# Kernel tuning notes

Measured on AMD Instinct MI355X. Metric: run time of the kernel, lower is better.

Reference implementation:

```python
import jax, jax.numpy as jnp
import numpy as np

B, L, D = 2, 1024, 1024
H = 16
NL = 2
DFF = 4 * D
EPS = 1e-5
W_SCALE = 0.02


def rmsnorm(x, w):
    # x * rsqrt(mean(x^2, -1) + eps) * w   (computed in fp32 as in the torch code)
    xf = x.astype(jnp.float32)
    n = xf * jax.lax.rsqrt(jnp.mean(xf * xf, axis=-1, keepdims=True) + EPS)
    return n.astype(x.dtype) * w


def setup_inputs() -> dict:
    key = jax.random.key(0)
    ks = jax.random.split(key, 10)
    x = jax.random.normal(ks[0], (B, L, D), dtype=jnp.float32)
    # torch nn.Linear weight layout: [out_features, in_features]; y = x @ W.T + b
    qw = jax.random.normal(ks[1], (NL, D, D), dtype=jnp.float32) * W_SCALE
    kw = jax.random.normal(ks[2], (NL, D, D), dtype=jnp.float32) * W_SCALE
    vw = jax.random.normal(ks[3], (NL, D, D), dtype=jnp.float32) * W_SCALE
    ow = jax.random.normal(ks[4], (NL, D, D), dtype=jnp.float32) * W_SCALE
    pn_w = jnp.ones((NL, D), dtype=jnp.float32)
    ln_w = jnp.ones((NL, D), dtype=jnp.float32)
    fc_w = jax.random.normal(ks[5], (NL, DFF, D), dtype=jnp.float32) * W_SCALE
    fc2_w = jax.random.normal(ks[6], (NL, D, DFF), dtype=jnp.float32) * W_SCALE
    fc2_b = jnp.zeros((NL, D), dtype=jnp.float32)
    return {"x": x, "qw": qw, "kw": kw, "vw": vw, "ow": ow,
            "pn_w": pn_w, "ln_w": ln_w, "fc_w": fc_w, "fc2_w": fc2_w, "fc2_b": fc2_b}


def reference(x, qw, kw, vw, ow, pn_w, ln_w, fc_w, fc2_w, fc2_b):
    d = D // H
    for i in range(NL):
        # --- LinearAttention block (dropout=0 -> identity) ---
        h = rmsnorm(x, pn_w[i])                                   # [B,L,D]
        Q = (h @ qw[i].T).reshape(B, L, H, d)
        K = (h @ kw[i].T).reshape(B, L, H, d)
        V = (h @ vw[i].T).reshape(B, L, H, d)
        # outer-product state per position, cumulated over L (causal linear attn)
        W = jnp.einsum('blhd,blhe->blhde', K, V)                  # [B,L,H,d,d]
        W = jnp.cumsum(W, axis=1)
        a = jnp.einsum('blhd,blhde->blhe', Q, W).reshape(B, L, D)
        x = x + a @ ow[i].T
        # --- MLP block ---
        m = rmsnorm(x, ln_w[i])
        f = jax.nn.gelu(m @ fc_w[i].T, approximate=False)         # torch nn.GELU default = exact
        x = x + f @ fc2_w[i].T + fc2_b[i]
    return x
```

## Files before the change

kernel.cpp:

```cpp
#include <hip/hip_runtime.h>

#define BB 2
#define LL 1024
#define DD 1024
#define HH 16
#define HD 64
#define DFFN 4096
#define MM (BB*LL)
#define QS 3072

using u16 = unsigned short;
typedef __bf16 bf16x8 __attribute__((ext_vector_type(8)));
typedef float f32x4 __attribute__((ext_vector_type(4)));

__device__ __forceinline__ float b2f(u16 u) {
  union { unsigned int i; float f; } v; v.i = ((unsigned int)u) << 16; return v.f;
}
__device__ __forceinline__ u16 f2b(float f) {
  union { float f; unsigned int i; } v; v.f = f;
  unsigned int x = v.i;
  return (u16)((x + 0x7fffu + ((x >> 16) & 1u)) >> 16);
}
__device__ __forceinline__ float gelu_exact(float x) {
  return 0.5f * x * (1.0f + erff(x * 0.70710678118654752f));
}
__device__ __forceinline__ void gl2lds16(const void* g, void* l) {
  __builtin_amdgcn_global_load_lds((const __attribute__((address_space(1))) void*)g,
                                   (__attribute__((address_space(3))) void*)l, 16, 0, 0);
}

__global__ __launch_bounds__(256) void castw_kernel(const float* __restrict__ in,
                                                    u16* __restrict__ out, int n8) {
  int i = blockIdx.x * 256 + threadIdx.x;
  if (i >= n8) return;
  const float4 a = reinterpret_cast<const float4*>(in)[2 * i];
  const float4 b = reinterpret_cast<const float4*>(in)[2 * i + 1];
  uint4 o;
  o.x = (unsigned)f2b(a.x) | ((unsigned)f2b(a.y) << 16);
  o.y = (unsigned)f2b(a.z) | ((unsigned)f2b(a.w) << 16);
  o.z = (unsigned)f2b(b.x) | ((unsigned)f2b(b.y) << 16);
  o.w = (unsigned)f2b(b.z) | ((unsigned)f2b(b.w) << 16);
  reinterpret_cast<uint4*>(out)[i] = o;
}
__global__ __launch_bounds__(256) void castw3_kernel(const float* __restrict__ s0,
                                                     const float* __restrict__ s1,
                                                     const float* __restrict__ s2,
                                                     u16* __restrict__ out, int n8) {
  int i = blockIdx.x * 256 + threadIdx.x;
  if (i >= n8) return;
  const float* in = (blockIdx.y == 0) ? s0 : (blockIdx.y == 1) ? s1 : s2;
  u16* dst = out + (size_t)blockIdx.y * n8 * 8;
  const float4 a = reinterpret_cast<const float4*>(in)[2 * i];
  const float4 b = reinterpret_cast<const float4*>(in)[2 * i + 1];
  uint4 o;
  o.x = (unsigned)f2b(a.x) | ((unsigned)f2b(a.y) << 16);
  o.y = (unsigned)f2b(a.z) | ((unsigned)f2b(a.w) << 16);
  o.z = (unsigned)f2b(b.x) | ((unsigned)f2b(b.y) << 16);
  o.w = (unsigned)f2b(b.z) | ((unsigned)f2b(b.w) << 16);
  reinterpret_cast<uint4*>(dst)[i] = o;
}

__global__ __launch_bounds__(256) void init_out_kernel(float* __restrict__ out,
                                                       const float* __restrict__ resid,
                                                       const float* __restrict__ bias) {
  const int i = blockIdx.x * 256 + threadIdx.x;
  float4 v = reinterpret_cast<const float4*>(resid)[i];
  if (bias != nullptr) {
    const float4 bv = *reinterpret_cast<const float4*>(bias + ((i * 4) & (DD - 1)));
    v.x += bv.x; v.y += bv.y; v.z += bv.z; v.w += bv.w;
  }
  reinterpret_cast<float4*>(out)[i] = v;
}

__global__ __launch_bounds__(256) void rmsnorm_kernel(const float* __restrict__ x,
                                                      const float* __restrict__ w,
                                                      u16* __restrict__ out) {
  const int row = blockIdx.x, t = threadIdx.x;
  const float4 v = reinterpret_cast<const float4*>(x + (size_t)row * DD)[t];
  float ss = v.x*v.x + v.y*v.y + v.z*v.z + v.w*v.w;
  #pragma unroll
  for (int o = 32; o > 0; o >>= 1) ss += __shfl_down(ss, o);
  __shared__ float red[4];
  if ((t & 63) == 0) red[t >> 6] = ss;
  __syncthreads();
  const float inv = rsqrtf((red[0] + red[1] + red[2] + red[3]) * (1.0f / DD) + 1e-5f);
  const float4 wv = reinterpret_cast<const float4*>(w)[t];
  ushort4 o;
  o.x = f2b(v.x * inv * wv.x);
  o.y = f2b(v.y * inv * wv.y);
  o.z = f2b(v.z * inv * wv.z);
  o.w = f2b(v.w * inv * wv.w);
  reinterpret_cast<ushort4*>(out + (size_t)row * DD)[t] = o;
}

template<int ROWS, int NT>
__device__ __forceinline__ void dma32(const u16* __restrict__ g, int r0, int K, int kt,
                                      int t, u16* lds) {
  #pragma unroll
  for (int i = 0; i < ROWS * 4 / NT; i++) {
    const int c = i * NT + t;
    gl2lds16(g + (size_t)(r0 + (c >> 2)) * K + kt + (c & 3) * 8, &lds[c * 8]);
  }
}
__device__ __forceinline__ void mfma_tile32(const u16* Asb, const u16* Bsb,
                                            int wm, int wn, int fr, int fq, f32x4 acc[4][4]) {
  bf16x8 af[4], bfv[4];
  #pragma unroll
  for (int i = 0; i < 4; i++)
    af[i] = *reinterpret_cast<const bf16x8*>(&Asb[(wm + i * 16 + fr) * 32 + fq * 8]);
  #pragma unroll
  for (int j = 0; j < 4; j++)
    bfv[j] = *reinterpret_cast<const bf16x8*>(&Bsb[(wn + j * 16 + fr) * 32 + fq * 8]);
  #pragma unroll
  for (int i = 0; i < 4; i++)
    #pragma unroll
    for (int j = 0; j < 4; j++)
      acc[i][j] = __builtin_amdgcn_mfma_f32_16x16x32_bf16(af[i], bfv[j], acc[i][j], 0, 0, 0);
}

template<int BM, int BN, int ACT>
__global__ __launch_bounds__((BM/64)*(BN/64)*64)
void mfma_gemm(const u16* __restrict__ A, const u16* __restrict__ Wb,
               u16* __restrict__ Cb, int N, int K) {
  constexpr int WCOLS = BN / 64;
  constexpr int NW = (BM / 64) * WCOLS;
  constexpr int NT = NW * 64;
  __shared__ u16 As[BM * 32];
  __shared__ u16 Bs[BN * 32];
  const int t = threadIdx.x;
  const int lane = t & 63, w = t >> 6;
  const int wm = (w / WCOLS) * 64, wn = (w % WCOLS) * 64;
  const int m0 = blockIdx.y * BM, n0 = blockIdx.x * BN;
  const int fr = lane & 15, fq = lane >> 4;

  f32x4 acc[4][4] = {};
  for (int kt = 0; kt < K; kt += 32) {
    dma32<BM, NT>(A, m0, K, kt, t, As);
    dma32<BN, NT>(Wb, n0, K, kt, t, Bs);
    __syncthreads();
    mfma_tile32(As, Bs, wm, wn, fr, fq, acc);
    __syncthreads();
  }

  #pragma unroll
  for (int i = 0; i < 4; i++)
    #pragma unroll
    for (int j = 0; j < 4; j++)
      #pragma unroll
      for (int r = 0; r < 4; r++) {
        const int row = m0 + wm + i * 16 + fq * 4 + r;
        const int col = n0 + wn + j * 16 + fr;
        float val = acc[i][j][r];
        if (ACT == 1) val = gelu_exact(val);
        Cb[(size_t)row * N + col] = f2b(val);
      }
}

template<int SPLIT>
__global__ __launch_bounds__(128)
void mfma_gemm_sk(const u16* __restrict__ A, const u16* __restrict__ Wb,
                  float* __restrict__ Co, int N, int K) {
  constexpr int BM = 128, BN = 64, NT = 128;
  __shared__ u16 As[BM * 32];
  __shared__ u16 Bs[BN * 32];
  const int t = threadIdx.x;
  const int lane = t & 63, w = t >> 6;
  const int wm = w * 64, wn = 0;
  const int m0 = blockIdx.y * BM, n0 = blockIdx.x * BN;
  const int fr = lane & 15, fq = lane >> 4;
  const int Kc = K / SPLIT, k0 = blockIdx.z * Kc, kend = k0 + Kc;

  f32x4 acc[4][4] = {};
  for (int kt = k0; kt < kend; kt += 32) {
    dma32<BM, NT>(A, m0, K, kt, t, As);
    dma32<BN, NT>(Wb, n0, K, kt, t, Bs);
    __syncthreads();
    mfma_tile32(As, Bs, wm, wn, fr, fq, acc);
    __syncthreads();
  }

  #pragma unroll
  for (int i = 0; i < 4; i++)
    #pragma unroll
    for (int j = 0; j < 4; j++)
      #pragma unroll
      for (int r = 0; r < 4; r++) {
        const int row = m0 + wm + i * 16 + fq * 4 + r;
        const int col = n0 + wn + j * 16 + fr;
        unsafeAtomicAdd(&Co[(size_t)row * N + col], acc[i][j][r]);
      }
}

__global__ __launch_bounds__(256) void kv_trans(const u16* __restrict__ QKV,
                                                u16* __restrict__ Kt, u16* __restrict__ Vt) {
  __shared__ u16 T[64][72];
  const int tile = blockIdx.x;
  const int h2 = blockIdx.y;
  const int b = blockIdx.z;
  const int h = h2 & 15, which = h2 >> 4;
  const int t = threadIdx.x;
  const int pos = t >> 2, d0 = (t & 3) * 16;
  const u16* src = QKV + ((size_t)(b * LL) + tile * 64 + pos) * QS + 1024 + which * 1024 + h * HD + d0;
  union { uint4 u[2]; u16 s[16]; } pk;
  pk.u[0] = reinterpret_cast<const uint4*>(src)[0];
  pk.u[1] = reinterpret_cast<const uint4*>(src)[1];
  #pragma unroll
  for (int j = 0; j < 16; j++) T[d0 + j][pos] = pk.s[j];
  __syncthreads();
  const int d = t >> 2, p0 = (t & 3) * 16;
  u16* dst = (which ? Vt : Kt) + ((size_t)(b * HH + h) * HD + d) * LL + tile * 64 + p0;
  union { uint4 u[2]; u16 s[16]; } ok;
  #pragma unroll
  for (int j = 0; j < 16; j++) ok.s[j] = T[d][p0 + j];
  reinterpret_cast<uint4*>(dst)[0] = ok.u[0];
  reinterpret_cast<uint4*>(dst)[1] = ok.u[1];
}

__global__ __launch_bounds__(256) void attn_phase1(const u16* __restrict__ QKV,
                                                   const u16* __restrict__ Kt,
                                                   const u16* __restrict__ Vt,
                                                   u16* __restrict__ Oa,
                                                   u16* __restrict__ Slt) {
  __shared__ u16 Ss[4][16][64];
  const int tile = blockIdx.x, h = blockIdx.y, b = blockIdx.z;
  const int t = threadIdx.x, lane = t & 63, w = t >> 6;
  const int fr = lane & 15, fq = lane >> 4;
  const size_t tok0 = (size_t)(b * LL + tile * 64);
  const size_t bh = (size_t)(b * HH + h);
  const u16* Qb  = QKV + tok0 * QS + h * HD;
  const u16* Kb  = Qb + 1024;
  const u16* Ktb = Kt + bh * (HD * LL) + tile * 64;
  const u16* Vtb = Vt + bh * (HD * LL) + tile * 64;

  bf16x8 aq[2], bk[4][2];
  #pragma unroll
  for (int kh = 0; kh < 2; kh++)
    aq[kh] = *reinterpret_cast<const bf16x8*>(Qb + (size_t)(16*w + fr) * QS + kh*32 + fq*8);
  #pragma unroll
  for (int n4 = 0; n4 < 4; n4++)
    #pragma unroll
    for (int kh = 0; kh < 2; kh++)
      bk[n4][kh] = *reinterpret_cast<const bf16x8*>(Kb + (size_t)(16*n4 + fr) * QS + kh*32 + fq*8);
  f32x4 sacc[4] = {};
  #pragma unroll
  for (int n4 = 0; n4 < 4; n4++) {
    sacc[n4] = __builtin_amdgcn_mfma_f32_16x16x32_bf16(aq[0], bk[n4][0], sacc[n4], 0, 0, 0);
    sacc[n4] = __builtin_amdgcn_mfma_f32_16x16x32_bf16(aq[1], bk[n4][1], sacc[n4], 0, 0, 0);
  }
  #pragma unroll
  for (int n4 = 0; n4 < 4; n4++)
    #pragma unroll
    for (int r = 0; r < 4; r++) {
      const bool keep = (16*w + 4*fq + r) >= (16*n4 + fr);
      Ss[w][4*fq + r][16*n4 + fr] = keep ? f2b(sacc[n4][r]) : (u16)0;
    }
  __syncthreads();

  bf16x8 va[2], kt[4][2];
  #pragma unroll
  for (int kh = 0; kh < 2; kh++)
    va[kh] = *reinterpret_cast<const bf16x8*>(Vtb + (size_t)(16*w + fr) * LL + kh*32 + fq*8);
  #pragma unroll
  for (int n4 = 0; n4 < 4; n4++)
    #pragma unroll
    for (int kh = 0; kh < 2; kh++)
      kt[n4][kh] = *reinterpret_cast<const bf16x8*>(Ktb + (size_t)(16*n4 + fr) * LL + kh*32 + fq*8);
  f32x4 lacc[4] = {};
  #pragma unroll
  for (int n4 = 0; n4 < 4; n4++) {
    lacc[n4] = __builtin_amdgcn_mfma_f32_16x16x32_bf16(va[0], kt[n4][0], lacc[n4], 0, 0, 0);
    lacc[n4] = __builtin_amdgcn_mfma_f32_16x16x32_bf16(va[1], kt[n4][1], lacc[n4], 0, 0, 0);
  }
  u16* So = Slt + (bh * 16 + tile) * 4096;
  #pragma unroll
  for (int n4 = 0; n4 < 4; n4++)
    #pragma unroll
    for (int r = 0; r < 4; r++)
      So[(size_t)(16*w + 4*fq + r) * 64 + 16*n4 + fr] = f2b(lacc[n4][r]);

  bf16x8 sa[2], vb[4][2];
  #pragma unroll
  for (int kh = 0; kh < 2; kh++)
    sa[kh] = *reinterpret_cast<const bf16x8*>(&Ss[w][fr][kh*32 + fq*8]);
  #pragma unroll
  for (int n4 = 0; n4 < 4; n4++)
    #pragma unroll
    for (int kh = 0; kh < 2; kh++)
      vb[n4][kh] = *reinterpret_cast<const bf16x8*>(Vtb + (size_t)(16*n4 + fr) * LL + kh*32 + fq*8);
  f32x4 oacc[4] = {};
  #pragma unroll
  for (int n4 = 0; n4 < 4; n4++) {
    oacc[n4] = __builtin_amdgcn_mfma_f32_16x16x32_bf16(sa[0], vb[n4][0], oacc[n4], 0, 0, 0);
    oacc[n4] = __builtin_amdgcn_mfma_f32_16x16x32_bf16(sa[1], vb[n4][1], oacc[n4], 0, 0, 0);
  }
  u16* Ob = Oa + (tok0 + 16*w) * DD + h * HD;
  #pragma unroll
  for (int n4 = 0; n4 < 4; n4++)
    #pragma unroll
    for (int r = 0; r < 4; r++)
      Ob[(size_t)(4*fq + r) * DD + 16*n4 + fr] = f2b(oacc[n4][r]);
}

__global__ __launch_bounds__(256) void attn_phase2(const u16* __restrict__ Slt,
                                                   u16* __restrict__ Wc) {
  const int rg = blockIdx.x, h = blockIdx.y, b = blockIdx.z;
  const size_t base = ((size_t)((b * HH + h) * 16)) * 4096 + rg * 512 + threadIdx.x * 2;
  float r0 = 0.f, r1 = 0.f;
  for (int tl = 0; tl < 16; tl++) {
    const size_t p = base + (size_t)tl * 4096;
    const unsigned d = *reinterpret_cast<const unsigned*>(Slt + p);
    *reinterpret_cast<unsigned*>(Wc + p) = (unsigned)f2b(r0) | ((unsigned)f2b(r1) << 16);
    r0 += b2f((u16)(d & 0xffff));
    r1 += b2f((u16)(d >> 16));
  }
}

__global__ __launch_bounds__(256) void attn_phase3(const u16* __restrict__ QKV,
                                                   const u16* __restrict__ Wc,
                                                   u16* __restrict__ Oa) {
  const int tile = blockIdx.x, h = blockIdx.y, b = blockIdx.z;
  const int t = threadIdx.x, lane = t & 63, w = t >> 6;
  const int fr = lane & 15, fq = lane >> 4;
  const size_t tok0 = (size_t)(b * LL + tile * 64);
  const size_t bh = (size_t)(b * HH + h);
  const u16* Qb = QKV + tok0 * QS + h * HD;
  const u16* Wb = Wc + (bh * 16 + tile) * 4096;

  bf16x8 aq[2], wb[4][2];
  #pragma unroll
  for (int kh = 0; kh < 2; kh++)
    aq[kh] = *reinterpret_cast<const bf16x8*>(Qb + (size_t)(16*w + fr) * QS + kh*32 + fq*8);
  #pragma unroll
  for (int n4 = 0; n4 < 4; n4++)
    #pragma unroll
    for (int kh = 0; kh < 2; kh++)
      wb[n4][kh] = *reinterpret_cast<const bf16x8*>(Wb + (size_t)(16*n4 + fr) * 64 + kh*32 + fq*8);
  f32x4 oacc[4] = {};
  #pragma unroll
  for (int n4 = 0; n4 < 4; n4++) {
    oacc[n4] = __builtin_amdgcn_mfma_f32_16x16x32_bf16(aq[0], wb[n4][0], oacc[n4], 0, 0, 0);
    oacc[n4] = __builtin_amdgcn_mfma_f32_16x16x32_bf16(aq[1], wb[n4][1], oacc[n4], 0, 0, 0);
  }
  u16* Ob = Oa + (tok0 + 16*w) * DD + h * HD;
  #pragma unroll
  for (int n4 = 0; n4 < 4; n4++)
    #pragma unroll
    for (int r = 0; r < 4; r++) {
      const size_t idx = (size_t)(4*fq + r) * DD + 16*n4 + fr;
      Ob[idx] = f2b(b2f(Ob[idx]) + oacc[n4][r]);
    }
}

extern "C" void kernel_launch(void* const* d_in, const int* in_sizes, int n_in,
                              void* d_out, int out_size, void* d_ws, size_t ws_size,
                              hipStream_t stream) {
  const float* x_in = (const float*)d_in[0];
  const float* qw   = (const float*)d_in[1];
  const float* kw   = (const float*)d_in[2];
  const float* vw   = (const float*)d_in[3];
  const float* ow   = (const float*)d_in[4];
  const float* pn   = (const float*)d_in[5];
  const float* ln   = (const float*)d_in[6];
  const float* fcw  = (const float*)d_in[7];
  const float* fc2w = (const float*)d_in[8];
  const float* fc2b = (const float*)d_in[9];

  char* ws = (char*)d_ws;
  u16* wbuf = (u16*)ws;
  u16* slt  = (u16*)ws;
  u16* wcum = (u16*)(ws + (size_t)(4 << 20));
  u16* h    = (u16*)(ws + (size_t)(8 << 20));
  u16* qkv  = (u16*)(ws + (size_t)(12 << 20));
  u16* f    = (u16*)(ws + (size_t)(12 << 20));
  u16* vt   = (u16*)(ws + (size_t)(24 << 20));
  u16* kt   = (u16*)(ws + (size_t)(28 << 20));
  float* xf = (float*)d_out;

  const int n8D = DD * DD / 8;
  const int n8F = DFFN * DD / 8;
  const int gInit = MM * DD / 4 / 256;

  for (int i = 0; i < 2; i++) {
    const float* qwi  = qw   + (size_t)i * DD * DD;
    const float* kwi  = kw   + (size_t)i * DD * DD;
    const float* vwi  = vw   + (size_t)i * DD * DD;
    const float* owi  = ow   + (size_t)i * DD * DD;
    const float* fcwi = fcw  + (size_t)i * DFFN * DD;
    const float* f2wi = fc2w + (size_t)i * DD * DFFN;
    const float* src  = (i == 0) ? x_in : xf;

    rmsnorm_kernel<<<MM, 256, 0, stream>>>(src, pn + i * DD, h);
    castw3_kernel<<<dim3(n8D / 256, 3), 256, 0, stream>>>(qwi, kwi, vwi, wbuf, n8D);
    mfma_gemm<128, 64, 0><<<dim3(QS / 64, MM / 128), 128, 0, stream>>>(
        h, wbuf, qkv, QS, DD);
    kv_trans<<<dim3(16, 32, BB), 256, 0, stream>>>(qkv, kt, vt);
    attn_phase1<<<dim3(16, HH, BB), 256, 0, stream>>>(qkv, kt, vt, h, slt);
    attn_phase2<<<dim3(8, HH, BB), 256, 0, stream>>>(slt, wcum);
    attn_phase3<<<dim3(16, HH, BB), 256, 0, stream>>>(qkv, wcum, h);
    castw_kernel<<<n8D / 256, 256, 0, stream>>>(owi, wbuf, n8D);
    init_out_kernel<<<gInit, 256, 0, stream>>>(xf, src, nullptr);
    mfma_gemm_sk<2><<<dim3(DD / 64, MM / 128, 2), 128, 0, stream>>>(h, wbuf, xf, DD, DD);
    rmsnorm_kernel<<<MM, 256, 0, stream>>>(xf, ln + i * DD, h);
    castw_kernel<<<n8F / 256, 256, 0, stream>>>(fcwi, wbuf, n8F);
    mfma_gemm<128, 64, 1><<<dim3(DFFN / 64, MM / 128), 128, 0, stream>>>(
        h, wbuf, f, DFFN, DD);
    castw_kernel<<<n8F / 256, 256, 0, stream>>>(f2wi, wbuf, n8F);
    float* co = (i == 1) ? (float*)d_out : xf;
    init_out_kernel<<<gInit, 256, 0, stream>>>(co, xf, fc2b + i * DD);
    mfma_gemm_sk<4><<<dim3(DD / 64, MM / 128, 4), 128, 0, stream>>>(f, wbuf, co, DD, DFFN);
  }
}
```

Before: 536.1 us.

## Double-buffer GEMM shared-memory tiles and enlarge MLP GEMM tiles to 128x128

Adds LDS double buffering to both GEMM kernels: the next K-slice is fetched into the alternate buffer while MFMAs run on the current one, and one barrier per iteration is removed. The split-K kernel is templated on tile shape, and the two MLP GEMMs move to 128x128 tiles with 256 threads for more operand reuse. The cost is twice the shared memory and fewer blocks for the FC1 and FC2 grids, which may lower occupancy.

```diff
diff --git a/kernel.cpp b/kernel.cpp
--- a/kernel.cpp
+++ b/kernel.cpp
@@ -125,8 +125,8 @@
   constexpr int WCOLS = BN / 64;
   constexpr int NW = (BM / 64) * WCOLS;
   constexpr int NT = NW * 64;
-  __shared__ u16 As[BM * 32];
-  __shared__ u16 Bs[BN * 32];
+  __shared__ u16 As[2][BM * 32];
+  __shared__ u16 Bs[2][BN * 32];
   const int t = threadIdx.x;
   const int lane = t & 63, w = t >> 6;
   const int wm = (w / WCOLS) * 64, wn = (w % WCOLS) * 64;
@@ -134,12 +134,18 @@
   const int fr = lane & 15, fq = lane >> 4;
 
   f32x4 acc[4][4] = {};
+  dma32<BM, NT>(A, m0, K, 0, t, As[0]);
+  dma32<BN, NT>(Wb, n0, K, 0, t, Bs[0]);
+  __syncthreads();
+  int p = 0;
   for (int kt = 0; kt < K; kt += 32) {
-    dma32<BM, NT>(A, m0, K, kt, t, As);
-    dma32<BN, NT>(Wb, n0, K, kt, t, Bs);
+    if (kt + 32 < K) {
+      dma32<BM, NT>(A, m0, K, kt + 32, t, As[p ^ 1]);
+      dma32<BN, NT>(Wb, n0, K, kt + 32, t, Bs[p ^ 1]);
+    }
+    mfma_tile32(As[p], Bs[p], wm, wn, fr, fq, acc);
     __syncthreads();
-    mfma_tile32(As, Bs, wm, wn, fr, fq, acc);
-    __syncthreads();
+    p ^= 1;
   }
 
   #pragma unroll
@@ -156,27 +162,35 @@
       }
 }
 
-template<int SPLIT>
-__global__ __launch_bounds__(128)
+template<int BM, int BN, int SPLIT>
+__global__ __launch_bounds__((BM/64)*(BN/64)*64)
 void mfma_gemm_sk(const u16* __restrict__ A, const u16* __restrict__ Wb,
                   float* __restrict__ Co, int N, int K) {
-  constexpr int BM = 128, BN = 64, NT = 128;
-  __shared__ u16 As[BM * 32];
-  __shared__ u16 Bs[BN * 32];
+  constexpr int WCOLS = BN / 64;
+  constexpr int NW = (BM / 64) * WCOLS;
+  constexpr int NT = NW * 64;
+  __shared__ u16 As[2][BM * 32];
+  __shared__ u16 Bs[2][BN * 32];
   const int t = threadIdx.x;
   const int lane = t & 63, w = t >> 6;
-  const int wm = w * 64, wn = 0;
+  const int wm = (w / WCOLS) * 64, wn = (w % WCOLS) * 64;
   const int m0 = blockIdx.y * BM, n0 = blockIdx.x * BN;
   const int fr = lane & 15, fq = lane >> 4;
   const int Kc = K / SPLIT, k0 = blockIdx.z * Kc, kend = k0 + Kc;
 
   f32x4 acc[4][4] = {};
+  dma32<BM, NT>(A, m0, K, k0, t, As[0]);
+  dma32<BN, NT>(Wb, n0, K, k0, t, Bs[0]);
+  __syncthreads();
+  int p = 0;
   for (int kt = k0; kt < kend; kt += 32) {
-    dma32<BM, NT>(A, m0, K, kt, t, As);
-    dma32<BN, NT>(Wb, n0, K, kt, t, Bs);
+    if (kt + 32 < kend) {
+      dma32<BM, NT>(A, m0, K, kt + 32, t, As[p ^ 1]);
+      dma32<BN, NT>(Wb, n0, K, kt + 32, t, Bs[p ^ 1]);
+    }
+    mfma_tile32(As[p], Bs[p], wm, wn, fr, fq, acc);
     __syncthreads();
-    mfma_tile32(As, Bs, wm, wn, fr, fq, acc);
-    __syncthreads();
+    p ^= 1;
   }
 
   #pragma unroll
@@ -399,14 +413,16 @@
     attn_phase3<<<dim3(16, HH, BB), 256, 0, stream>>>(qkv, wcum, h);
     castw_kernel<<<n8D / 256, 256, 0, stream>>>(owi, wbuf, n8D);
     init_out_kernel<<<gInit, 256, 0, stream>>>(xf, src, nullptr);
-    mfma_gemm_sk<2><<<dim3(DD / 64, MM / 128, 2), 128, 0, stream>>>(h, wbuf, xf, DD, DD);
+    mfma_gemm_sk<128, 64, 2><<<dim3(DD / 64, MM / 128, 2), 128, 0, stream>>>(
+        h, wbuf, xf, DD, DD);
     rmsnorm_kernel<<<MM, 256, 0, stream>>>(xf, ln + i * DD, h);
     castw_kernel<<<n8F / 256, 256, 0, stream>>>(fcwi, wbuf, n8F);
-    mfma_gemm<128, 64, 1><<<dim3(DFFN / 64, MM / 128), 128, 0, stream>>>(
+    mfma_gemm<128, 128, 1><<<dim3(DFFN / 128, MM / 128), 256, 0, stream>>>(
         h, wbuf, f, DFFN, DD);
     castw_kernel<<<n8F / 256, 256, 0, stream>>>(f2wi, wbuf, n8F);
     float* co = (i == 1) ? (float*)d_out : xf;
     init_out_kernel<<<gInit, 256, 0, stream>>>(co, xf, fc2b + i * DD);
-    mfma_gemm_sk<4><<<dim3(DD / 64, MM / 128, 4), 128, 0, stream>>>(f, wbuf, co, DD, DFFN);
-  }
-}
+    mfma_gemm_sk<128, 128, 4><<<dim3(DD / 128, MM / 128, 4), 256, 0, stream>>>(
+        f, wbuf, co, DD, DFFN);
+  }
+}
```

New measurement: 514.8 us. 4.0% less time.
